# Kernel tuning notes

Hardware: AMD Instinct MI355X
Metric: run time of the kernel (lower is better)

Reference implementation:

```python
import jax, jax.numpy as jnp
import numpy as np

N_HEADS = 16
D_HEAD = 64


def setup_inputs() -> dict:
    key = jax.random.key(0)
    ks = jax.random.split(key, 9)
    B, L, D = 2, 2048, 1024
    s = 0.02  # small init scale for weights
    return {
        "x": jax.random.normal(ks[0], (B, L, D), jnp.float32),
        "Wq": jax.random.normal(ks[1], (D, D), jnp.float32) * s,
        "bq": jax.random.normal(ks[2], (D,), jnp.float32) * s,
        "Wk": jax.random.normal(ks[3], (D, D), jnp.float32) * s,
        "bk": jax.random.normal(ks[4], (D,), jnp.float32) * s,
        "Wv": jax.random.normal(ks[5], (D, D), jnp.float32) * s,
        "bv": jax.random.normal(ks[6], (D,), jnp.float32) * s,
        "Wo": jax.random.normal(ks[7], (D, D), jnp.float32) * s,
        "bo": jax.random.normal(ks[8], (D,), jnp.float32) * s,
    }


def _alibi_bias(L, n_heads, dtype):
    # slopes m_i = 1 / x**(i+1), x = (2**8)**(1/n_heads)
    x = (2.0 ** 8) ** (1.0 / n_heads)
    slopes = jnp.asarray([1.0 / x ** (i + 1) for i in range(n_heads)], dtype=dtype)
    pos = jnp.arange(L)
    rel = (pos[None, :] - pos[:, None]).astype(dtype)  # [L, L], (j - i)
    return slopes[:, None, None] * rel[None, :, :]      # [H, L, L]


def reference(x, Wq, bq, Wk, bk, Wv, bv, Wo, bo):
    B, L, D = x.shape
    H, dh = N_HEADS, D_HEAD
    scale = dh ** -0.5
    q = (x @ Wq + bq).reshape(B, L, H, dh)
    k = (x @ Wk + bk).reshape(B, L, H, dh)
    v = (x @ Wv + bv).reshape(B, L, H, dh)
    scores = jnp.einsum("blhd,bmhd->bhlm", q, k) * scale  # [B,H,L,L]
    bias = _alibi_bias(L, H, scores.dtype)                 # [H,L,L]
    attn = jax.nn.softmax(scores + bias[None], axis=-1)
    out = jnp.einsum("bhlm,bmhd->blhd", attn, v).reshape(B, L, D)
    return out @ Wo + bo
```

## Files before the change

### kernel.cpp

```cpp
#include <hip/hip_runtime.h>
#include <cstdint>
#include <cstddef>

typedef unsigned short u16;
typedef unsigned int u32;
typedef __bf16 bf16x8 __attribute__((ext_vector_type(8)));
typedef float f32x4 __attribute__((ext_vector_type(4)));
typedef u32 u32x2 __attribute__((ext_vector_type(2)));
typedef unsigned short u16x8 __attribute__((ext_vector_type(8)));
typedef short s16x4 __attribute__((ext_vector_type(4)));

__device__ __forceinline__ u16 f2bf(float f) {
    u32 u = __float_as_uint(f);
    u += 0x7fffu + ((u >> 16) & 1u);
    return (u16)(u >> 16);
}

__device__ __forceinline__ float fexp2(float x) {
    float r;
    asm("v_exp_f32 %0, %1" : "=v"(r) : "v"(x));
    return r;
}

__device__ __forceinline__ void gl16(const void* g, void* l) {
    __builtin_amdgcn_global_load_lds(
        (const __attribute__((address_space(1))) unsigned int*)g,
        (__attribute__((address_space(3))) unsigned int*)l, 16, 0, 0);
}

__global__ __launch_bounds__(256) void cvt_x_k(const float* __restrict__ x,
                                               u16* __restrict__ o) {
    int i = blockIdx.x * 256 + threadIdx.x;
    const float4* xv = (const float4*)x;
    float4 a = xv[2 * i], b = xv[2 * i + 1];
    ushort4 r0, r1;
    r0.x = f2bf(a.x); r0.y = f2bf(a.y); r0.z = f2bf(a.z); r0.w = f2bf(a.w);
    r1.x = f2bf(b.x); r1.y = f2bf(b.y); r1.z = f2bf(b.z); r1.w = f2bf(b.w);
    ((ushort4*)o)[2 * i] = r0;
    ((ushort4*)o)[2 * i + 1] = r1;
}

__global__ __launch_bounds__(256) void cvt_wT4_k(const float* __restrict__ Wq,
                                                 const float* __restrict__ Wk,
                                                 const float* __restrict__ Wv,
                                                 const float* __restrict__ Wo,
                                                 u16* __restrict__ oqkv,
                                                 u16* __restrict__ oo) {
    __shared__ float tile[64][65];
    const int z = blockIdx.z;
    const float* W = (z == 0) ? Wq : (z == 1) ? Wk : (z == 2) ? Wv : Wo;
    u16* o = (z < 3) ? (oqkv + ((size_t)z << 20)) : oo;
    const int bx = blockIdx.x, by = blockIdx.y;
    const int t = threadIdx.x, tn = t & 63, tr = t >> 6;
#pragma unroll
    for (int r = 0; r < 16; ++r) {
        int kk = r * 4 + tr;
        tile[kk][tn] = W[(size_t)(by * 64 + kk) * 1024 + bx * 64 + tn];
    }
    __syncthreads();
#pragma unroll
    for (int r = 0; r < 16; ++r) {
        int nn = r * 4 + tr;
        o[(size_t)(bx * 64 + nn) * 1024 + by * 64 + tn] = f2bf(tile[tn][nn]);
    }
}

template <int MODE>
__global__ __launch_bounds__(256) void gemm_k(
    const u16* __restrict__ A, const u16* __restrict__ Bt,
    const float* __restrict__ bias0, const float* __restrict__ bias1,
    const float* __restrict__ bias2,
    u16* __restrict__ oq, u16* __restrict__ ok_, u16* __restrict__ ov,
    float* __restrict__ oc) {
    __shared__ __align__(16) u16 As[3 * 128 * 32];
    __shared__ __align__(16) u16 Bs[3 * 128 * 32];
    const int t = threadIdx.x, w = t >> 6, lane = t & 63;
    const int lr = lane & 15, lg = lane >> 4;
    const int brow = blockIdx.x * 128, bcol = blockIdx.y * 128;
    const int wr = w >> 1, wc = w & 1;
    const char* Ab = (const char*)A + (size_t)brow * 2048;
    const char* Bb = (const char*)Bt + (size_t)bcol * 2048;
    const int lrow = lane >> 2;
    const int lcol = (((lane & 3) ^ ((lane >> 3) & 3)) << 4);
    const int r0a = w * 32, r0b = w * 32 + 16;
    const size_t ga = (size_t)(r0a + lrow) * 2048 + lcol;
    const size_t gb = (size_t)(r0b + lrow) * 2048 + lcol;
    const int rsw = ((lg ^ ((lr >> 1) & 3)) << 4);

    f32x4 acc[4][4];
#pragma unroll
    for (int m = 0; m < 4; ++m)
#pragma unroll
        for (int n = 0; n < 4; ++n) acc[m][n] = (f32x4){0.f, 0.f, 0.f, 0.f};

    gl16(Ab + ga, (char*)As + r0a * 64);
    gl16(Ab + gb, (char*)As + r0b * 64);
    gl16(Bb + ga, (char*)Bs + r0a * 64);
    gl16(Bb + gb, (char*)Bs + r0b * 64);
    gl16(Ab + ga + 64, (char*)As + 8192 + r0a * 64);
    gl16(Ab + gb + 64, (char*)As + 8192 + r0b * 64);
    gl16(Bb + ga + 64, (char*)Bs + 8192 + r0a * 64);
    gl16(Bb + gb + 64, (char*)Bs + 8192 + r0b * 64);

    for (int tt = 0; tt < 32; ++tt) {
        if (tt < 31) {
            asm volatile("s_waitcnt vmcnt(4)" ::: "memory");
        } else {
            asm volatile("s_waitcnt vmcnt(0)" ::: "memory");
        }
        __builtin_amdgcn_s_barrier();
        __builtin_amdgcn_sched_barrier(0);
        if (tt < 30) {
            const int nb = (tt + 2) % 3;
            const size_t ko = (size_t)(tt + 2) * 64;
            char* Asn = (char*)As + nb * 8192;
            char* Bsn = (char*)Bs + nb * 8192;
            gl16(Ab + ga + ko, Asn + r0a * 64);
            gl16(Ab + gb + ko, Asn + r0b * 64);
            gl16(Bb + ga + ko, Bsn + r0a * 64);
            gl16(Bb + gb + ko, Bsn + r0b * 64);
        }
        const char* AsB = (const char*)As + (tt % 3) * 8192;
        const char* BsB = (const char*)Bs + (tt % 3) * 8192;
        bf16x8 af[4], bfr[4];
#pragma unroll
        for (int m = 0; m < 4; ++m)
            af[m] = *(const bf16x8*)(AsB + (wr * 64 + m * 16 + lr) * 64 + rsw);
#pragma unroll
        for (int n = 0; n < 4; ++n)
            bfr[n] = *(const bf16x8*)(BsB + (wc * 64 + n * 16 + lr) * 64 + rsw);
#pragma unroll
        for (int m = 0; m < 4; ++m)
#pragma unroll
            for (int n = 0; n < 4; ++n)
                acc[m][n] = __builtin_amdgcn_mfma_f32_16x16x32_bf16(af[m], bfr[n],
                                                                    acc[m][n], 0, 0, 0);
    }

    const float QSCALE = 0.125f * 1.44269504f;
#pragma unroll
    for (int n = 0; n < 4; ++n) {
        const int col = bcol + wc * 64 + n * 16 + lr;
        if (MODE == 0) {
#pragma unroll
            for (int m = 0; m < 4; ++m)
#pragma unroll
                for (int r = 0; r < 4; ++r) {
                    int row = brow + wr * 64 + m * 16 + 4 * lg + r;
                    int b = row >> 11, l = row & 2047;
                    float val = acc[m][n][r];
                    if (col < 1024) {
                        int hh = col >> 6, d = col & 63;
                        oq[(((size_t)b * 16 + hh) * 2048 + l) * 64 + d] =
                            f2bf((val + bias0[col]) * QSCALE);
                    } else if (col < 2048) {
                        int c = col - 1024, hh = c >> 6, d = c & 63;
                        ok_[(((size_t)b * 16 + hh) * 2048 + l) * 64 + d] =
                            f2bf(val + bias1[c]);
                    } else {
                        int c = col - 2048, hh = c >> 6, d = c & 63;
                        ov[(((size_t)b * 16 + hh) * 64 + d) * 2048 + l] =
                            f2bf(val + bias2[c]);
                    }
                }
        } else {
            const float bb = bias0[col];
#pragma unroll
            for (int m = 0; m < 4; ++m)
#pragma unroll
                for (int r = 0; r < 4; ++r) {
                    int row = brow + wr * 64 + m * 16 + 4 * lg + r;
                    oc[(size_t)row * 1024 + col] = acc[m][n][r] + bb;
                }
        }
    }
}

__global__ __launch_bounds__(256, 2) void attn_k(const u16* __restrict__ qg_,
                                                 const u16* __restrict__ kg_,
                                                 const u16* __restrict__ vg_,
                                                 u16* __restrict__ ao) {
    __shared__ __align__(16) u16 smem[32768];
    char* Kbase = (char*)smem;
    char* Vbase = (char*)smem + 32768;
    const int t = threadIdx.x, w = t >> 6, lane = t & 63;
    const int lr = lane & 15, lg = lane >> 4;
    const int bid = blockIdx.y * 16 + blockIdx.x;
    const int qt = (bid >> 3) & 15;
    const int bh = ((bid >> 7) << 3) | (bid & 7);
    const int q0 = qt * 128, h = bh & 15, bb = bh >> 4;
    const float sl2 = exp2f(-0.5f * (float)(h + 1)) * 1.44269504f;

    const char* khead = (const char*)(kg_ + (size_t)bh * 2048 * 64);
    const char* vhead = (const char*)(vg_ + (size_t)bh * 64 * 2048);

    const int krow = lane >> 3, ku = lane & 7;
    const int kso = (w * 32 + krow) * 128 + ((ku ^ (krow & 7)) << 4);
    const int kdo = w * 4096;
    const int vrow = lane >> 4, vgr = lane & 15;
    int vso[4];
#pragma unroll
    for (int i = 0; i < 4; ++i)
        vso[i] = (w * 16 + 4 * i + vrow) * 4096 +
                 ((vgr ^ ((4 * i + vrow) & 7)) << 4);
    const int vdo = w * 4096;

    const char* qpA = (const char*)qg_ +
                      ((size_t)bh * 2048 + q0 + w * 32 + lr) * 128;
    bf16x8 qa0A = *(const bf16x8*)(qpA + lg * 16);
    bf16x8 qa1A = *(const bf16x8*)(qpA + 64 + lg * 16);
    bf16x8 qa0B = *(const bf16x8*)(qpA + 2048 + lg * 16);
    bf16x8 qa1B = *(const bf16x8*)(qpA + 2048 + 64 + lg * 16);

    f32x4 abF2[8];
#pragma unroll
    for (int n = 0; n < 8; ++n)
#pragma unroll
        for (int r = 0; r < 4; ++r)
            abF2[n][r] = sl2 * (float)(n * 16 + 4 * lg + r - 2047) - 16.0f;
    const float ainc = sl2 * 128.0f;
    f32x4 oaccA[4], oaccB[4];
#pragma unroll
    for (int nn = 0; nn < 4; ++nn) {
        oaccA[nn] = (f32x4){0.f, 0.f, 0.f, 0.f};
        oaccB[nn] = (f32x4){0.f, 0.f, 0.f, 0.f};
    }
    f32x4 laccA = (f32x4){0.f, 0.f, 0.f, 0.f};
    f32x4 laccB = (f32x4){0.f, 0.f, 0.f, 0.f};
    const u32x2 onesb = {0x3F803F80u, 0x3F803F80u};
    const s16x4 ones = __builtin_bit_cast(s16x4, onesb);

    {
        char* kd = Kbase + kdo;
        char* vd = Vbase + vdo;
#pragma unroll
        for (int i = 0; i < 4; ++i) gl16(khead + kso + i * 1024, kd + i * 1024);
#pragma unroll
        for (int i = 0; i < 4; ++i) gl16(vhead + vso[i], vd + i * 1024);
    }
    asm volatile("s_waitcnt vmcnt(0)" ::: "memory");
    __builtin_amdgcn_s_barrier();
    __builtin_amdgcn_sched_barrier(0);

    for (int tt = 0; tt < 16; ++tt) {
        if (tt < 15) {
            const char* ks = khead + (size_t)(tt + 1) * 16384;
            const char* vs = vhead + (size_t)(tt + 1) * 256;
            char* kd = Kbase + ((tt + 1) & 1) * 16384 + kdo;
            char* vd = Vbase + ((tt + 1) & 1) * 16384 + vdo;
#pragma unroll
            for (int i = 0; i < 4; ++i) gl16(ks + kso + i * 1024, kd + i * 1024);
#pragma unroll
            for (int i = 0; i < 4; ++i) gl16(vs + vso[i], vd + i * 1024);
        }
        const char* Kc = Kbase + (tt & 1) * 16384;
        const char* Vc = Vbase + (tt & 1) * 16384;

        f32x4 saA[8], saB[8];
        __builtin_amdgcn_s_setprio(1);
#pragma unroll
        for (int n = 0; n < 8; ++n) {
            bf16x8 kf = *(const bf16x8*)(Kc + (n * 16 + lr) * 128 +
                                         ((lg ^ (lr & 7)) << 4));
            saA[n] = __builtin_amdgcn_mfma_f32_16x16x32_bf16(kf, qa0A, abF2[n],
                                                             0, 0, 0);
            saB[n] = __builtin_amdgcn_mfma_f32_16x16x32_bf16(kf, qa0B, abF2[n],
                                                             0, 0, 0);
        }
#pragma unroll
        for (int n = 0; n < 8; ++n) {
            bf16x8 kf = *(const bf16x8*)(Kc + (n * 16 + lr) * 128 +
                                         (((4 + lg) ^ (lr & 7)) << 4));
            saA[n] = __builtin_amdgcn_mfma_f32_16x16x32_bf16(kf, qa1A, saA[n],
                                                             0, 0, 0);
            saB[n] = __builtin_amdgcn_mfma_f32_16x16x32_bf16(kf, qa1B, saB[n],
                                                             0, 0, 0);
        }
        __builtin_amdgcn_s_setprio(0);

#pragma unroll
        for (int n = 0; n < 8; ++n)
#pragma unroll
            for (int r = 0; r < 4; ++r) {
                saA[n][r] = fexp2(saA[n][r]);
                saB[n][r] = fexp2(saB[n][r]);
            }
#pragma unroll
        for (int n = 0; n < 8; ++n) abF2[n] += ainc;

        __builtin_amdgcn_s_setprio(1);
#pragma unroll
        for (int n = 0; n < 8; ++n) {
            u32 lo, hi;
            asm("v_cvt_pk_bf16_f32 %0, %1, %2"
                : "=v"(lo) : "v"(saA[n][0]), "v"(saA[n][1]));
            asm("v_cvt_pk_bf16_f32 %0, %1, %2"
                : "=v"(hi) : "v"(saA[n][2]), "v"(saA[n][3]));
            u32x2 tmpa = {lo, hi};
            s16x4 pnA = __builtin_bit_cast(s16x4, tmpa);
            asm("v_cvt_pk_bf16_f32 %0, %1, %2"
                : "=v"(lo) : "v"(saB[n][0]), "v"(saB[n][1]));
            asm("v_cvt_pk_bf16_f32 %0, %1, %2"
                : "=v"(hi) : "v"(saB[n][2]), "v"(saB[n][3]));
            u32x2 tmpb = {lo, hi};
            s16x4 pnB = __builtin_bit_cast(s16x4, tmpb);
            laccA = __builtin_amdgcn_mfma_f32_16x16x16bf16_1k(ones, pnA,
                                                              laccA, 0, 0, 0);
            laccB = __builtin_amdgcn_mfma_f32_16x16x16bf16_1k(ones, pnB,
                                                              laccB, 0, 0, 0);
#pragma unroll
            for (int nn = 0; nn < 4; ++nn) {
                s16x4 va = *(const s16x4*)(Vc + (nn * 16 + lr) * 256 +
                                           (((2 * n + (lg >> 1)) ^ (lr & 7)) << 4) +
                                           ((lg & 1) << 3));
                oaccA[nn] = __builtin_amdgcn_mfma_f32_16x16x16bf16_1k(va, pnA,
                                                                      oaccA[nn],
                                                                      0, 0, 0);
                oaccB[nn] = __builtin_amdgcn_mfma_f32_16x16x16bf16_1k(va, pnB,
                                                                      oaccB[nn],
                                                                      0, 0, 0);
            }
        }
        __builtin_amdgcn_s_setprio(0);

        asm volatile("s_waitcnt vmcnt(0)" ::: "memory");
        __builtin_amdgcn_s_barrier();
        __builtin_amdgcn_sched_barrier(0);
    }

    const float linvA = 1.0f / laccA[0];
    const float linvB = 1.0f / laccB[0];
    u16* ow = smem + w * (32 * 72);
#pragma unroll
    for (int nn = 0; nn < 4; ++nn)
#pragma unroll
        for (int r = 0; r < 4; ++r) {
            ow[lr * 72 + nn * 16 + 4 * lg + r] = f2bf(oaccA[nn][r] * linvA);
            ow[(16 + lr) * 72 + nn * 16 + 4 * lg + r] = f2bf(oaccB[nn][r] * linvB);
        }
    __syncthreads();
    const int q_ = lane >> 2, d0 = (lane & 3) << 4;
    const u16* orowA = smem + w * (32 * 72) + q_ * 72 + d0;
    const u16* orowB = orowA + 16 * 72;
    u16x8 a0 = *(const u16x8*)(orowA);
    u16x8 a1 = *(const u16x8*)(orowA + 8);
    u16x8 b0 = *(const u16x8*)(orowB);
    u16x8 b1 = *(const u16x8*)(orowB + 8);
    size_t gaddr = ((size_t)bb * 2048 + q0 + w * 32 + q_) * 1024 + h * 64 + d0;
    *(u16x8*)(ao + gaddr) = a0;
    *(u16x8*)(ao + gaddr + 8) = a1;
    *(u16x8*)(ao + gaddr + 16 * 1024) = b0;
    *(u16x8*)(ao + gaddr + 16 * 1024 + 8) = b1;
}

extern "C" void kernel_launch(void* const* d_in, const int* in_sizes, int n_in,
                              void* d_out, int out_size, void* d_ws, size_t ws_size,
                              hipStream_t stream) {
    const float* x  = (const float*)d_in[0];
    const float* Wq = (const float*)d_in[1];
    const float* bq = (const float*)d_in[2];
    const float* Wk = (const float*)d_in[3];
    const float* bk = (const float*)d_in[4];
    const float* Wv = (const float*)d_in[5];
    const float* bv = (const float*)d_in[6];
    const float* Wo = (const float*)d_in[7];
    const float* bo = (const float*)d_in[8];

    const size_t MB = 1u << 20;
    if (ws_size < 40 * MB) return;
    char* ws = (char*)d_ws;
    u16* xb    = (u16*)(ws);
    u16* wqkvt = (u16*)(ws + 8 * MB);
    u16* wot   = (u16*)(ws + 14 * MB);
    u16* qb    = (u16*)(ws + 16 * MB);
    u16* kb    = (u16*)(ws + 24 * MB);
    u16* vt    = (u16*)(ws + 32 * MB);
    u16* ao    = xb;

    cvt_x_k<<<2048, 256, 0, stream>>>(x, xb);
    cvt_wT4_k<<<dim3(16, 16, 4), 256, 0, stream>>>(Wq, Wk, Wv, Wo, wqkvt, wot);

    gemm_k<0><<<dim3(32, 24), 256, 0, stream>>>(xb, wqkvt, bq, bk, bv,
                                                qb, kb, vt, nullptr);
    attn_k<<<dim3(16, 32), 256, 0, stream>>>(qb, kb, vt, ao);
    gemm_k<1><<<dim3(32, 8), 256, 0, stream>>>(ao, wot, bo, nullptr, nullptr,
                                               nullptr, nullptr, nullptr,
                                               (float*)d_out);
}
```

Measured before the change: 127.5 us.

## Merge conversion kernels and stage transposed V epilogue through LDS

```diff
diff --git a/kernel.cpp b/kernel.cpp
--- a/kernel.cpp
+++ b/kernel.cpp
@@ -28,30 +28,32 @@
         (__attribute__((address_space(3))) unsigned int*)l, 16, 0, 0);
 }
 
-__global__ __launch_bounds__(256) void cvt_x_k(const float* __restrict__ x,
-                                               u16* __restrict__ o) {
-    int i = blockIdx.x * 256 + threadIdx.x;
-    const float4* xv = (const float4*)x;
-    float4 a = xv[2 * i], b = xv[2 * i + 1];
-    ushort4 r0, r1;
-    r0.x = f2bf(a.x); r0.y = f2bf(a.y); r0.z = f2bf(a.z); r0.w = f2bf(a.w);
-    r1.x = f2bf(b.x); r1.y = f2bf(b.y); r1.z = f2bf(b.z); r1.w = f2bf(b.w);
-    ((ushort4*)o)[2 * i] = r0;
-    ((ushort4*)o)[2 * i + 1] = r1;
-}
-
-__global__ __launch_bounds__(256) void cvt_wT4_k(const float* __restrict__ Wq,
+__global__ __launch_bounds__(256) void cvt_all_k(const float* __restrict__ Wq,
                                                  const float* __restrict__ Wk,
                                                  const float* __restrict__ Wv,
                                                  const float* __restrict__ Wo,
+                                                 const float* __restrict__ x,
                                                  u16* __restrict__ oqkv,
-                                                 u16* __restrict__ oo) {
+                                                 u16* __restrict__ oo,
+                                                 u16* __restrict__ ox) {
+    const int z = blockIdx.z;
+    const int bx = blockIdx.x, by = blockIdx.y;
+    const int t = threadIdx.x;
+    if (z >= 4) {
+        int i = ((z - 4) * 256 + by * 16 + bx) * 256 + t;
+        const float4* xv = (const float4*)x;
+        float4 a = xv[2 * i], b = xv[2 * i + 1];
+        ushort4 r0, r1;
+        r0.x = f2bf(a.x); r0.y = f2bf(a.y); r0.z = f2bf(a.z); r0.w = f2bf(a.w);
+        r1.x = f2bf(b.x); r1.y = f2bf(b.y); r1.z = f2bf(b.z); r1.w = f2bf(b.w);
+        ((ushort4*)ox)[2 * i] = r0;
+        ((ushort4*)ox)[2 * i + 1] = r1;
+        return;
+    }
     __shared__ float tile[64][65];
-    const int z = blockIdx.z;
     const float* W = (z == 0) ? Wq : (z == 1) ? Wk : (z == 2) ? Wv : Wo;
     u16* o = (z < 3) ? (oqkv + ((size_t)z << 20)) : oo;
-    const int bx = blockIdx.x, by = blockIdx.y;
-    const int t = threadIdx.x, tn = t & 63, tr = t >> 6;
+    const int tn = t & 63, tr = t >> 6;
 #pragma unroll
     for (int r = 0; r < 16; ++r) {
         int kk = r * 4 + tr;
@@ -72,8 +74,9 @@
     const float* __restrict__ bias2,
     u16* __restrict__ oq, u16* __restrict__ ok_, u16* __restrict__ ov,
     float* __restrict__ oc) {
-    __shared__ __align__(16) u16 As[3 * 128 * 32];
-    __shared__ __align__(16) u16 Bs[3 * 128 * 32];
+    __shared__ __align__(16) u16 sh[2 * 3 * 128 * 32];
+    u16* As = sh;
+    u16* Bs = sh + 3 * 128 * 32;
     const int t = threadIdx.x, w = t >> 6, lane = t & 63;
     const int lr = lane & 15, lg = lane >> 4;
     const int brow = blockIdx.x * 128, bcol = blockIdx.y * 128;
@@ -138,6 +141,31 @@
     }
 
     const float QSCALE = 0.125f * 1.44269504f;
+    if (MODE == 0 && bcol >= 2048) {
+        const int b = brow >> 11, l0 = brow & 2047;
+        __syncthreads();
+#pragma unroll
+        for (int n = 0; n < 4; ++n) {
+            const int cl = wc * 64 + n * 16 + lr;
+            const float bb2 = bias2[bcol - 2048 + cl];
+#pragma unroll
+            for (int m = 0; m < 4; ++m)
+#pragma unroll
+                for (int r = 0; r < 4; ++r) {
+                    int ll = wr * 64 + m * 16 + 4 * lg + r;
+                    sh[cl * 136 + ll] = f2bf(acc[m][n][r] + bb2);
+                }
+        }
+        __syncthreads();
+        const int rr = t >> 1, hf = t & 1;
+        const u16* src = sh + rr * 136 + hf * 64;
+        u16* dst = ov + ((size_t)b * 1024 + (bcol - 2048) + rr) * 2048 +
+                   l0 + hf * 64;
+#pragma unroll
+        for (int i = 0; i < 8; ++i)
+            *(u16x8*)(dst + i * 8) = *(const u16x8*)(src + i * 8);
+        return;
+    }
 #pragma unroll
     for (int n = 0; n < 4; ++n) {
         const int col = bcol + wc * 64 + n * 16 + lr;
@@ -153,14 +181,10 @@
                         int hh = col >> 6, d = col & 63;
                         oq[(((size_t)b * 16 + hh) * 2048 + l) * 64 + d] =
                             f2bf((val + bias0[col]) * QSCALE);
-                    } else if (col < 2048) {
+                    } else {
                         int c = col - 1024, hh = c >> 6, d = c & 63;
                         ok_[(((size_t)b * 16 + hh) * 2048 + l) * 64 + d] =
                             f2bf(val + bias1[c]);
-                    } else {
-                        int c = col - 2048, hh = c >> 6, d = c & 63;
-                        ov[(((size_t)b * 16 + hh) * 64 + d) * 2048 + l] =
-                            f2bf(val + bias2[c]);
                     }
                 }
         } else {
@@ -377,8 +401,8 @@
     u16* vt    = (u16*)(ws + 32 * MB);
     u16* ao    = xb;
 
-    cvt_x_k<<<2048, 256, 0, stream>>>(x, xb);
-    cvt_wT4_k<<<dim3(16, 16, 4), 256, 0, stream>>>(Wq, Wk, Wv, Wo, wqkvt, wot);
+    cvt_all_k<<<dim3(16, 16, 12), 256, 0, stream>>>(Wq, Wk, Wv, Wo, x,
+                                                    wqkvt, wot, xb);
 
     gemm_k<0><<<dim3(32, 24), 256, 0, stream>>>(xb, wqkvt, bq, bk, bv,
                                                 qb, kb, vt, nullptr);
```

Measured after the change: 113.3 us. -11.1%, faster.
